# Kernel tuning notes

Hardware: AMD Instinct MI355X
Metric: run time of the kernel (lower is better)

Reference implementation:

```python
import jax, jax.numpy as jnp
import numpy as np

KAPPA = -1.0          # negative curvature (Poincare ball, c = 1)
EPS = 1e-10
N, D_IN, D_OUT = 8192, 512, 512


def _artan_k(x):
    sc = np.sqrt(-KAPPA)
    return jnp.arctanh(jnp.clip(sc * x, -1.0 + 1e-7, 1.0 - 1e-7)) / sc


def _tan_k(x):
    sc = np.sqrt(-KAPPA)
    return jnp.tanh(sc * x) / sc


def _clamp_abs(x, eps=EPS):
    return jnp.where(x >= 0, 1.0, -1.0) * jnp.maximum(jnp.abs(x), eps)


def _norm(x):
    # stable last-dim L2 norm, clamped away from zero
    return jnp.sqrt(jnp.maximum(jnp.sum(x * x, axis=-1, keepdims=True), EPS * EPS))


def mobius_matvec(W, x):
    # geoopt-style Mobius matrix-vector product: scale x@W so that the
    # gyro-norm matches tan_k((|mx|/|x|) * artan_k(|x|))
    x_norm = _norm(x)                       # [N,1]
    mx = x @ W                              # [N,D_out]
    mx_norm = _norm(mx)
    res = _tan_k(mx_norm / x_norm * _artan_k(x_norm)) * (mx / mx_norm)
    return jnp.where(mx_norm <= EPS, 0.0, res)


def mobius_scalar_mul(r, x):
    x_norm = _norm(x)
    return _tan_k(r * _artan_k(x_norm)) * (x / x_norm)


def weighted_midpoint_lincomb(A, X):
    # weighted Frechet-mean-like midpoint with lincomb=True (geoopt semantics):
    # gamma_i = lambda_x = 2 / (1 + kappa * |x_i|^2)
    gamma = jnp.maximum(2.0 / (1.0 + KAPPA * jnp.sum(X * X, axis=-1, keepdims=True)), 1e-15)  # [N,1]
    denom = _clamp_abs(A @ (gamma - 1.0))   # [N,1]  (sum_j A_ij (gamma_j - 1))
    nom = A @ (gamma * X)                   # [N,D]  (sum_j A_ij gamma_j x_j)  -- GEMM, no NxNxD temp
    two_mean = nom / denom
    sq = jnp.sum(two_mean * two_mean, axis=-1, keepdims=True)
    a_mean = two_mean / (1.0 + jnp.sqrt(jnp.maximum(1.0 + KAPPA * sq, EPS)))
    alpha = jnp.sum(A, axis=-1, keepdims=True)   # lincomb: Mobius-scale by total weight
    return mobius_scalar_mul(alpha, a_mean)


def logmap0(x):
    xn = _norm(x)
    return _artan_k(xn) * x / xn


def expmap0(u):
    un = _norm(u)
    return _tan_k(un) * u / un


def setup_inputs() -> dict:
    key = jax.random.key(0)
    k1, k2, k3 = jax.random.split(key, 3)
    # node embeddings well inside the Poincare ball (|x| ~ 0.02)
    X = jax.random.normal(k1, (N, D_IN), dtype=jnp.float32) * 0.001
    # dense nonnegative normalized adjacency (rows sum ~ 0.5)
    A_hat = jax.random.uniform(k2, (N, N), dtype=jnp.float32) / N
    W = jax.random.normal(k3, (D_IN, D_OUT), dtype=jnp.float32) * 0.01
    return {"X": X, "A_hat": A_hat, "W": W}


def reference(X, A_hat, W):
    XW = mobius_matvec(W, X)                     # Mobius linear layer
    AXW = weighted_midpoint_lincomb(A_hat, XW)   # adjacency-weighted midpoint aggregation
    return expmap0(jax.nn.relu(logmap0(AXW)))    # sigma = exp0(relu(log0(.)))
```

## Files before the change

kernel.cpp:

```cpp
#include <hip/hip_runtime.h>


#define NR 8192
#define DD 512

typedef unsigned int u32;
typedef unsigned short u16;
typedef __attribute__((ext_vector_type(8))) short bf16x8;
typedef __attribute__((ext_vector_type(4))) float f32x4;

__device__ __forceinline__ u16 f2bf(float f) {
  u32 u = __float_as_uint(f);
  u32 r = u + 0x7FFFu + ((u >> 16) & 1u);
  return (u16)(r >> 16);
}

__device__ __forceinline__ u32 cvtpk(float lo, float hi) {
  u32 r;
  asm("v_cvt_pk_bf16_f32 %0, %1, %2" : "=v"(r) : "v"(lo), "v"(hi));
  return r;
}

__device__ __forceinline__ void gload16(const void* g, void* l) {
  __builtin_amdgcn_global_load_lds(
      (const __attribute__((address_space(1))) u32*)g,
      (__attribute__((address_space(3))) u32*)l, 16, 0, 0);
}

__device__ __forceinline__ float wred(float v) {
  #pragma unroll
  for (int off = 32; off; off >>= 1) v += __shfl_xor(v, off, 64);
  return v;
}

__global__ __launch_bounds__(256) void conv_wt(const float* __restrict__ W,
                                               u16* __restrict__ Wt) {
  const int idx = blockIdx.x * 256 + threadIdx.x;
  const int n  = idx >> 6;
  const int k0 = (idx & 63) * 8;
  u32 r[4];
  #pragma unroll
  for (int j = 0; j < 4; ++j) {
    float lo = W[(size_t)(k0 + 2*j    ) * DD + n];
    float hi = W[(size_t)(k0 + 2*j + 1) * DD + n];
    r[j] = (u32)f2bf(lo) | ((u32)f2bf(hi) << 16);
  }
  const int dst = n * DD + ((idx & 63) >> 2) * 32 + (((idx & 3) ^ (n & 3)) * 8);
  *(uint4*)(Wt + dst) = *(const uint4*)r;
}

template <int DOSUM>
__global__ __launch_bounds__(256, 2) void gemm_ph(
    const float* __restrict__ Af, const u16* __restrict__ Bt,
    const u16* __restrict__ g1bf,
    float* __restrict__ C0, float* __restrict__ Cext,
    float* __restrict__ denp, float* __restrict__ alp,
    int M, int K, int kchunk, int nkc) {
  __shared__ __align__(16) float ldsA[2][4096];
  __shared__ __align__(16) u16   ldsB[2][8192];
  __shared__ __align__(16) u16   ldsG[4096];

  const int bid = blockIdx.x;
  int mt, nt, kc;
  if (nkc == 4) {
    kc = (bid >> 1) & 3;
    nt = (bid >> 3) & 1;
    mt = ((bid >> 4) << 1) | (bid & 1);
  } else {
    kc = 0;
    nt = bid & 1;
    mt = bid >> 1;
  }

  const int t = threadIdx.x;
  const int lane = t & 63, w = t >> 6;
  const int wm = w >> 1, wn = w & 1;
  const int m0 = mt * 128, n0 = nt * 256;
  const int kbeg = kc * kchunk;
  const int lr = lane & 15, lk = lane >> 4, lx = lr & 7;
  const bool doRS = DOSUM && (nt == 0);

  const int scol = ((t & 7) ^ ((t >> 3) & 7)) << 2;
  const float* gA0 = Af + (size_t)(m0 + (t >> 3)) * K + kbeg + scol;
  const u16* gB = Bt + (size_t)(n0 + (t >> 2)) * K + kbeg + (t & 3) * 8;

  auto stage = [&](int buf, int kt) {
    const int ko = kt * 32;
    #pragma unroll
    for (int j = 0; j < 4; ++j)
      gload16(gA0 + ko + (size_t)j * 32 * K, &ldsA[buf][t * 4 + j * 1024]);
    #pragma unroll
    for (int j = 0; j < 4; ++j)
      gload16(gB + ko + (size_t)j * 64 * K, &ldsB[buf][t * 8 + j * 2048]);
  };

  f32x4 acc[4][8];
  #pragma unroll
  for (int i = 0; i < 4; ++i)
    #pragma unroll
    for (int j = 0; j < 8; ++j) acc[i][j] = (f32x4){0.f, 0.f, 0.f, 0.f};
  f32x4 accS[4];
  #pragma unroll
  for (int i = 0; i < 4; ++i) accS[i] = (f32x4){0.f, 0.f, 0.f, 0.f};

  const int nT = kchunk / 32;

  if (doRS) {
    #pragma unroll
    for (int j = 0; j < 2; ++j)
      gload16(g1bf + kbeg + t * 8 + j * 2048, &ldsG[t * 8 + j * 2048]);
  }
  stage(0, 0);
  stage(1, 1);
  asm volatile("s_waitcnt vmcnt(8)" ::: "memory");
  __builtin_amdgcn_s_barrier();
  __builtin_amdgcn_sched_barrier(0);

  int cur = 0;
  for (int tt = 0; tt < nT; ++tt) {
    bf16x8 af[4], bv[8];
    #pragma unroll
    for (int i = 0; i < 4; ++i) {
      const int rbase = (wm * 64 + i * 16 + lr) * 32;
      f32x4 lo = *(const f32x4*)&ldsA[cur][rbase + (((2*lk    ) ^ lx) << 2)];
      f32x4 hi = *(const f32x4*)&ldsA[cur][rbase + (((2*lk + 1) ^ lx) << 2)];
      union { u32 u[4]; bf16x8 v; } pk;
      pk.u[0] = cvtpk(lo.x, lo.y); pk.u[1] = cvtpk(lo.z, lo.w);
      pk.u[2] = cvtpk(hi.x, hi.y); pk.u[3] = cvtpk(hi.z, hi.w);
      af[i] = pk.v;
    }
    #pragma unroll
    for (int i = 0; i < 8; ++i) {
      const int rb = (wn * 128 + i * 16 + lr) * 32 + ((lk ^ (lr & 3)) << 3);
      bv[i] = *(const bf16x8*)&ldsB[cur][rb];
    }
    __builtin_amdgcn_s_setprio(1);
    #pragma unroll
    for (int mi = 0; mi < 4; ++mi)
      #pragma unroll
      for (int ni = 0; ni < 4; ++ni)
        acc[mi][ni] = __builtin_amdgcn_mfma_f32_16x16x32_bf16(
            af[mi], bv[ni], acc[mi][ni], 0, 0, 0);
    __builtin_amdgcn_s_setprio(0);
    asm volatile("s_waitcnt lgkmcnt(0)" ::: "memory");
    __builtin_amdgcn_sched_barrier(0);
    __builtin_amdgcn_s_barrier();
    __builtin_amdgcn_sched_barrier(0);
    if (tt + 2 < nT) stage(cur, tt + 2);
    bf16x8 gv;
    if (doRS && wn == 0) {
      if (lr == 0) {
        gv = *(const bf16x8*)&ldsG[tt * 32 + lk * 8];
      } else {
        const short s = (lr == 1) ? (short)0x3F80 : (short)0;
        gv = (bf16x8){s, s, s, s, s, s, s, s};
      }
    }
    __builtin_amdgcn_sched_barrier(0);
    __builtin_amdgcn_s_setprio(1);
    #pragma unroll
    for (int mi = 0; mi < 4; ++mi)
      #pragma unroll
      for (int ni = 4; ni < 8; ++ni)
        acc[mi][ni] = __builtin_amdgcn_mfma_f32_16x16x32_bf16(
            af[mi], bv[ni], acc[mi][ni], 0, 0, 0);
    if (doRS && wn == 0) {
      #pragma unroll
      for (int i = 0; i < 4; ++i)
        accS[i] = __builtin_amdgcn_mfma_f32_16x16x32_bf16(
            af[i], gv, accS[i], 0, 0, 0);
    }
    __builtin_amdgcn_s_setprio(0);
    __builtin_amdgcn_sched_barrier(0);
    if (tt + 1 < nT) {
      if (tt + 3 < nT) {
        asm volatile("s_waitcnt vmcnt(8)" ::: "memory");
      } else {
        asm volatile("s_waitcnt vmcnt(0)" ::: "memory");
      }
      __builtin_amdgcn_s_barrier();
      __builtin_amdgcn_sched_barrier(0);
    }
    cur ^= 1;
  }

  if (doRS && wn == 0 && lr < 2) {
    float* dst = ((lr == 0) ? denp : alp) + (size_t)kc * M + m0 + wm * 64;
    #pragma unroll
    for (int i = 0; i < 4; ++i)
      #pragma unroll
      for (int v = 0; v < 4; ++v)
        dst[i * 16 + lk * 4 + v] = accS[i][v];
  }

  float* C = (kc == 0) ? C0 : (Cext + (size_t)(kc - 1) * M * DD);
  float* Cw = C + (size_t)(m0 + wm * 64 + lk * 4) * DD + n0 + wn * 128 + lr;
  #pragma unroll
  for (int mi = 0; mi < 4; ++mi)
    #pragma unroll
    for (int ni = 0; ni < 8; ++ni)
      #pragma unroll
      for (int v = 0; v < 4; ++v)
        Cw[(size_t)(mi * 16 + v) * DD + ni * 16] = acc[mi][ni][v];
}

__global__ __launch_bounds__(256) void rowstats(const float* __restrict__ X,
                                                const float* __restrict__ mx,
                                                float* __restrict__ fg,
                                                u16* __restrict__ g1bf) {
  const int row  = (blockIdx.x << 2) + (threadIdx.x >> 6);
  const int lane = threadIdx.x & 63;
  const float* xr = X  + (size_t)row * DD + lane * 8;
  const float* mr = mx + (size_t)row * DD + lane * 8;
  float4 a0 = *(const float4*)xr, a1 = *(const float4*)(xr + 4);
  float4 b0 = *(const float4*)mr, b1 = *(const float4*)(mr + 4);
  float sx = a0.x*a0.x + a0.y*a0.y + a0.z*a0.z + a0.w*a0.w
           + a1.x*a1.x + a1.y*a1.y + a1.z*a1.z + a1.w*a1.w;
  float sm = b0.x*b0.x + b0.y*b0.y + b0.z*b0.z + b0.w*b0.w
           + b1.x*b1.x + b1.y*b1.y + b1.z*b1.z + b1.w*b1.w;
  sx = wred(sx); sm = wred(sm);
  if (lane == 0) {
    float xn  = sqrtf(fmaxf(sx, 1e-20f));
    float mxn = sqrtf(fmaxf(sm, 1e-20f));
    float at  = atanhf(fminf(xn, 0.9999999f));
    float t_  = tanhf(mxn / xn * at);
    bool  z   = (mxn <= 1e-10f);
    float factor = z ? 0.f : t_ / mxn;
    float xwsq   = z ? 0.f : t_ * t_ * (sm / (mxn * mxn));
    float g = 2.f / (1.f - xwsq);
    g = fmaxf(g, 1e-15f);
    fg[row] = factor * g;
    g1bf[row] = f2bf(g - 1.f);
  }
}

__global__ __launch_bounds__(256) void build_bt(const float* __restrict__ mx,
                                                const float* __restrict__ fg,
                                                u16* __restrict__ Bt) {
  __shared__ float tile[64][65];
  const int j0 = blockIdx.x * 64, d0 = blockIdx.y * 64;
  const int t = threadIdx.x;
  const int r0 = t >> 4, c4 = (t & 15) * 4;
  #pragma unroll
  for (int p = 0; p < 4; ++p) {
    const int r = r0 + p * 16;
    const float s = fg[j0 + r];
    float4 v = *(const float4*)&mx[(size_t)(j0 + r) * DD + d0 + c4];
    tile[r][c4 + 0] = s * v.x; tile[r][c4 + 1] = s * v.y;
    tile[r][c4 + 2] = s * v.z; tile[r][c4 + 3] = s * v.w;
  }
  __syncthreads();
  const int dr = t >> 2, jc = (t & 3) * 16;
  u32 r[8];
  #pragma unroll
  for (int u = 0; u < 8; ++u) {
    float lo = tile[jc + 2 * u][dr];
    float hi = tile[jc + 2 * u + 1][dr];
    r[u] = (u32)f2bf(lo) | ((u32)f2bf(hi) << 16);
  }
  const int s0 = (jc >> 3) & 3;
  const int px = dr & 3;
  u32* rowp = (u32*)(Bt + (size_t)(d0 + dr) * NR + j0 + (jc & 32));
  *(uint4*)(rowp + ((s0 ^ px) * 4))       = *(const uint4*)&r[0];
  *(uint4*)(rowp + (((s0 + 1) ^ px) * 4)) = *(const uint4*)&r[4];
}

__global__ __launch_bounds__(256) void epilogue(const float* __restrict__ P0,
                                                const float* __restrict__ P1,
                                                const float* __restrict__ P2,
                                                const float* __restrict__ P3,
                                                const float* __restrict__ denp,
                                                const float* __restrict__ alp,
                                                float* __restrict__ out) {
  const int row  = (blockIdx.x << 2) + (threadIdx.x >> 6);
  const int lane = threadIdx.x & 63;
  const size_t ro = (size_t)row * DD + lane * 8;
  float4 n0 = *(const float4*)(P0 + ro), n1 = *(const float4*)(P0 + ro + 4);
  float4 a, b;
  a = *(const float4*)(P1 + ro); b = *(const float4*)(P1 + ro + 4);
  n0.x += a.x; n0.y += a.y; n0.z += a.z; n0.w += a.w;
  n1.x += b.x; n1.y += b.y; n1.z += b.z; n1.w += b.w;
  a = *(const float4*)(P2 + ro); b = *(const float4*)(P2 + ro + 4);
  n0.x += a.x; n0.y += a.y; n0.z += a.z; n0.w += a.w;
  n1.x += b.x; n1.y += b.y; n1.z += b.z; n1.w += b.w;
  a = *(const float4*)(P3 + ro); b = *(const float4*)(P3 + ro + 4);
  n0.x += a.x; n0.y += a.y; n0.z += a.z; n0.w += a.w;
  n1.x += b.x; n1.y += b.y; n1.z += b.z; n1.w += b.w;

  float de = 0.f, alpha = 0.f;
  #pragma unroll
  for (int kc = 0; kc < 4; ++kc) {
    de    += denp[kc * NR + row];
    alpha += alp [kc * NR + row];
  }
  de = (de >= 0.f ? 1.f : -1.f) * fmaxf(fabsf(de), 1e-10f);

  float v[8] = {n0.x / de, n0.y / de, n0.z / de, n0.w / de,
                n1.x / de, n1.y / de, n1.z / de, n1.w / de};
  float sq = 0.f;
  #pragma unroll
  for (int j = 0; j < 8; ++j) sq += v[j] * v[j];
  sq = wred(sq);
  float s1 = 1.f + sqrtf(fmaxf(1.f - sq, 1e-10f));
  float an = sqrtf(fmaxf(sq / (s1 * s1), 1e-20f));
  float t2 = tanhf(alpha * atanhf(fminf(an, 0.9999999f)));
  float f2 = t2 / (an * s1);
  float xsq = f2 * f2 * sq;
  float xn = sqrtf(fmaxf(xsq, 1e-20f));
  float lf = atanhf(fminf(xn, 0.9999999f)) / xn;
  float u[8]; float us = 0.f;
  #pragma unroll
  for (int j = 0; j < 8; ++j) {
    u[j] = fmaxf(lf * f2 * v[j], 0.f);
    us += u[j] * u[j];
  }
  us = wred(us);
  float un = sqrtf(fmaxf(us, 1e-20f));
  float ef = tanhf(un) / un;
  float o[8];
  #pragma unroll
  for (int j = 0; j < 8; ++j) o[j] = ef * u[j];
  float* orow = out + (size_t)row * DD + lane * 8;
  *(float4*)orow       = (float4){o[0], o[1], o[2], o[3]};
  *(float4*)(orow + 4) = (float4){o[4], o[5], o[6], o[7]};
}

extern "C" void kernel_launch(void* const* d_in, const int* in_sizes, int n_in,
                              void* d_out, int out_size, void* d_ws, size_t ws_size,
                              hipStream_t stream) {
  const float* X = (const float*)d_in[0];
  const float* A = (const float*)d_in[1];
  const float* W = (const float*)d_in[2];
  float* out = (float*)d_out;
  char* ws = (char*)d_ws;

  float* mx   = (float*)(ws);
  float* Pext = (float*)(ws + 16777216);
  u16*   Bt   = (u16*)(ws + 67108864);
  u16*   Wt   = (u16*)(ws + 75497472);
  float* fg   = (float*)(ws + 76021760);
  u16*   g1bf = (u16*)(ws + 76054528);
  float* denp = (float*)(ws + 76087296);
  float* alp  = (float*)(ws + 76218368);

  const size_t MNf = (size_t)NR * DD;

  conv_wt<<<128, 256, 0, stream>>>(W, Wt);
  gemm_ph<0><<<128, 256, 0, stream>>>(X, Wt, g1bf, mx, mx, denp, alp,
                                      NR, DD, DD, 1);
  rowstats<<<2048, 256, 0, stream>>>(X, mx, fg, g1bf);
  build_bt<<<dim3(128, 8), 256, 0, stream>>>(mx, fg, Bt);
  gemm_ph<1><<<512, 256, 0, stream>>>(A, Bt, g1bf, mx, Pext, denp, alp,
                                      NR, NR, NR / 4, 4);
  epilogue<<<2048, 256, 0, stream>>>(mx, Pext, Pext + MNf, Pext + 2 * MNf,
                                     denp, alp, out);
}
```

Measured before the change: 178.2 us.

## Load fp32 A operand directly into registers and shrink GEMM N-tile to 128

The GEMM kernel stops staging the fp32 A tile through LDS. Each lane now prefetches its own A fragments from global memory into registers, double-buffered, and converts them to bf16 just before the MFMAs. The N tile is halved from 256 to 128, so the grid doubles and the per-wave accumulator footprint and LDS use shrink, which should raise occupancy. In exchange, A is re-read from global memory by twice as many blocks, and the global A loads are less coalesced, 32-byte row segments per lane.

```diff
diff --git a/kernel.cpp b/kernel.cpp
--- a/kernel.cpp
+++ b/kernel.cpp
@@ -50,138 +50,137 @@
 }
 
 template <int DOSUM>
-__global__ __launch_bounds__(256, 2) void gemm_ph(
+__global__ __launch_bounds__(256, 2) void gemm_ra(
     const float* __restrict__ Af, const u16* __restrict__ Bt,
     const u16* __restrict__ g1bf,
     float* __restrict__ C0, float* __restrict__ Cext,
     float* __restrict__ denp, float* __restrict__ alp,
     int M, int K, int kchunk, int nkc) {
-  __shared__ __align__(16) float ldsA[2][4096];
-  __shared__ __align__(16) u16   ldsB[2][8192];
-  __shared__ __align__(16) u16   ldsG[4096];
+  __shared__ __align__(16) u16 ldsB[2][4096];
+  __shared__ __align__(16) u16 ldsG[2048];
 
   const int bid = blockIdx.x;
   int mt, nt, kc;
   if (nkc == 4) {
     kc = (bid >> 1) & 3;
-    nt = (bid >> 3) & 1;
-    mt = ((bid >> 4) << 1) | (bid & 1);
+    nt = (bid >> 3) & 3;
+    mt = ((bid >> 5) << 1) | (bid & 1);
   } else {
     kc = 0;
-    nt = bid & 1;
-    mt = bid >> 1;
+    nt = bid & 3;
+    mt = bid >> 2;
   }
 
   const int t = threadIdx.x;
   const int lane = t & 63, w = t >> 6;
   const int wm = w >> 1, wn = w & 1;
-  const int m0 = mt * 128, n0 = nt * 256;
+  const int m0 = mt * 128, n0 = nt * 128;
   const int kbeg = kc * kchunk;
-  const int lr = lane & 15, lk = lane >> 4, lx = lr & 7;
+  const int lr = lane & 15, lk = lane >> 4;
   const bool doRS = DOSUM && (nt == 0);
-
-  const int scol = ((t & 7) ^ ((t >> 3) & 7)) << 2;
-  const float* gA0 = Af + (size_t)(m0 + (t >> 3)) * K + kbeg + scol;
+  const int nT = kchunk / 32;
+
+  const float* aP[4];
+  #pragma unroll
+  for (int i = 0; i < 4; ++i)
+    aP[i] = Af + (size_t)(m0 + wm * 64 + i * 16 + lr) * K + kbeg + lk * 8;
+
   const u16* gB = Bt + (size_t)(n0 + (t >> 2)) * K + kbeg + (t & 3) * 8;
 
-  auto stage = [&](int buf, int kt) {
-    const int ko = kt * 32;
-    #pragma unroll
-    for (int j = 0; j < 4; ++j)
-      gload16(gA0 + ko + (size_t)j * 32 * K, &ldsA[buf][t * 4 + j * 1024]);
-    #pragma unroll
-    for (int j = 0; j < 4; ++j)
-      gload16(gB + ko + (size_t)j * 64 * K, &ldsB[buf][t * 8 + j * 2048]);
+  float4 pa0[4], pa1[4], pb0[4], pb1[4];
+  auto refill = [&](float4 (&d0)[4], float4 (&d1)[4]) {
+    #pragma unroll
+    for (int i = 0; i < 4; ++i) {
+      d0[i] = *(const float4*)(aP[i]);
+      d1[i] = *(const float4*)(aP[i] + 4);
+      aP[i] += 32;
+    }
   };
 
-  f32x4 acc[4][8];
+  f32x4 acc[4][4];
   #pragma unroll
   for (int i = 0; i < 4; ++i)
     #pragma unroll
-    for (int j = 0; j < 8; ++j) acc[i][j] = (f32x4){0.f, 0.f, 0.f, 0.f};
+    for (int j = 0; j < 4; ++j) acc[i][j] = (f32x4){0.f, 0.f, 0.f, 0.f};
   f32x4 accS[4];
   #pragma unroll
   for (int i = 0; i < 4; ++i) accS[i] = (f32x4){0.f, 0.f, 0.f, 0.f};
 
-  const int nT = kchunk / 32;
-
-  if (doRS) {
-    #pragma unroll
-    for (int j = 0; j < 2; ++j)
-      gload16(g1bf + kbeg + t * 8 + j * 2048, &ldsG[t * 8 + j * 2048]);
-  }
-  stage(0, 0);
-  stage(1, 1);
-  asm volatile("s_waitcnt vmcnt(8)" ::: "memory");
+  if (doRS) gload16(g1bf + kbeg + t * 8, &ldsG[t * 8]);
+  refill(pa0, pa1);
+  refill(pb0, pb1);
+  #pragma unroll
+  for (int j = 0; j < 2; ++j)
+    gload16(gB + (size_t)j * 64 * K, &ldsB[0][t * 8 + j * 2048]);
+  #pragma unroll
+  for (int j = 0; j < 2; ++j)
+    gload16(gB + 32 + (size_t)j * 64 * K, &ldsB[1][t * 8 + j * 2048]);
+  asm volatile("s_waitcnt vmcnt(2)" ::: "memory");
   __builtin_amdgcn_s_barrier();
   __builtin_amdgcn_sched_barrier(0);
 
-  int cur = 0;
-  for (int tt = 0; tt < nT; ++tt) {
-    bf16x8 af[4], bv[8];
+  auto subiter = [&](int T, float4 (&P0)[4], float4 (&P1)[4], u16* bbuf) {
+    bf16x8 bv[4];
+    #pragma unroll
+    for (int i = 0; i < 4; ++i)
+      bv[i] = *(const bf16x8*)
+          &bbuf[(wn * 64 + i * 16 + lr) * 32 + ((lk ^ (lr & 3)) << 3)];
+    bf16x8 gvv;
+    if (doRS && wn == 0) {
+      if (lr == 0) {
+        gvv = *(const bf16x8*)&ldsG[T * 32 + lk * 8];
+      } else {
+        const short s = (lr == 1) ? (short)0x3F80 : (short)0;
+        gvv = (bf16x8){s, s, s, s, s, s, s, s};
+      }
+    }
+    bf16x8 af[4];
     #pragma unroll
     for (int i = 0; i < 4; ++i) {
-      const int rbase = (wm * 64 + i * 16 + lr) * 32;
-      f32x4 lo = *(const f32x4*)&ldsA[cur][rbase + (((2*lk    ) ^ lx) << 2)];
-      f32x4 hi = *(const f32x4*)&ldsA[cur][rbase + (((2*lk + 1) ^ lx) << 2)];
       union { u32 u[4]; bf16x8 v; } pk;
-      pk.u[0] = cvtpk(lo.x, lo.y); pk.u[1] = cvtpk(lo.z, lo.w);
-      pk.u[2] = cvtpk(hi.x, hi.y); pk.u[3] = cvtpk(hi.z, hi.w);
+      pk.u[0] = cvtpk(P0[i].x, P0[i].y); pk.u[1] = cvtpk(P0[i].z, P0[i].w);
+      pk.u[2] = cvtpk(P1[i].x, P1[i].y); pk.u[3] = cvtpk(P1[i].z, P1[i].w);
       af[i] = pk.v;
     }
-    #pragma unroll
-    for (int i = 0; i < 8; ++i) {
-      const int rb = (wn * 128 + i * 16 + lr) * 32 + ((lk ^ (lr & 3)) << 3);
-      bv[i] = *(const bf16x8*)&ldsB[cur][rb];
-    }
-    __builtin_amdgcn_s_setprio(1);
-    #pragma unroll
-    for (int mi = 0; mi < 4; ++mi)
-      #pragma unroll
-      for (int ni = 0; ni < 4; ++ni)
-        acc[mi][ni] = __builtin_amdgcn_mfma_f32_16x16x32_bf16(
-            af[mi], bv[ni], acc[mi][ni], 0, 0, 0);
-    __builtin_amdgcn_s_setprio(0);
+    const bool more = (T + 2 < nT);
+    if (more) refill(P0, P1);
     asm volatile("s_waitcnt lgkmcnt(0)" ::: "memory");
     __builtin_amdgcn_sched_barrier(0);
     __builtin_amdgcn_s_barrier();
     __builtin_amdgcn_sched_barrier(0);
-    if (tt + 2 < nT) stage(cur, tt + 2);
-    bf16x8 gv;
-    if (doRS && wn == 0) {
-      if (lr == 0) {
-        gv = *(const bf16x8*)&ldsG[tt * 32 + lk * 8];
-      } else {
-        const short s = (lr == 1) ? (short)0x3F80 : (short)0;
-        gv = (bf16x8){s, s, s, s, s, s, s, s};
-      }
+    if (more) {
+      const size_t ko = (size_t)(T + 2) * 32;
+      #pragma unroll
+      for (int j = 0; j < 2; ++j)
+        gload16(gB + ko + (size_t)j * 64 * K, &bbuf[t * 8 + j * 2048]);
     }
     __builtin_amdgcn_sched_barrier(0);
     __builtin_amdgcn_s_setprio(1);
     #pragma unroll
     for (int mi = 0; mi < 4; ++mi)
       #pragma unroll
-      for (int ni = 4; ni < 8; ++ni)
+      for (int ni = 0; ni < 4; ++ni)
         acc[mi][ni] = __builtin_amdgcn_mfma_f32_16x16x32_bf16(
             af[mi], bv[ni], acc[mi][ni], 0, 0, 0);
     if (doRS && wn == 0) {
       #pragma unroll
       for (int i = 0; i < 4; ++i)
         accS[i] = __builtin_amdgcn_mfma_f32_16x16x32_bf16(
-            af[i], gv, accS[i], 0, 0, 0);
+            af[i], gvv, accS[i], 0, 0, 0);
     }
     __builtin_amdgcn_s_setprio(0);
     __builtin_amdgcn_sched_barrier(0);
-    if (tt + 1 < nT) {
-      if (tt + 3 < nT) {
-        asm volatile("s_waitcnt vmcnt(8)" ::: "memory");
-      } else {
-        asm volatile("s_waitcnt vmcnt(0)" ::: "memory");
-      }
+    if (T + 1 < nT) {
+      if (more) asm volatile("s_waitcnt vmcnt(10)" ::: "memory");
+      else      asm volatile("s_waitcnt vmcnt(0)"  ::: "memory");
       __builtin_amdgcn_s_barrier();
       __builtin_amdgcn_sched_barrier(0);
     }
-    cur ^= 1;
+  };
+
+  for (int tt = 0; tt < nT; tt += 2) {
+    subiter(tt,     pa0, pa1, &ldsB[0][0]);
+    subiter(tt + 1, pb0, pb1, &ldsB[1][0]);
   }
 
   if (doRS && wn == 0 && lr < 2) {
@@ -194,11 +193,11 @@
   }
 
   float* C = (kc == 0) ? C0 : (Cext + (size_t)(kc - 1) * M * DD);
-  float* Cw = C + (size_t)(m0 + wm * 64 + lk * 4) * DD + n0 + wn * 128 + lr;
+  float* Cw = C + (size_t)(m0 + wm * 64 + lk * 4) * DD + n0 + wn * 64 + lr;
   #pragma unroll
   for (int mi = 0; mi < 4; ++mi)
     #pragma unroll
-    for (int ni = 0; ni < 8; ++ni)
+    for (int ni = 0; ni < 4; ++ni)
       #pragma unroll
       for (int v = 0; v < 4; ++v)
         Cw[(size_t)(mi * 16 + v) * DD + ni * 16] = acc[mi][ni][v];
@@ -346,12 +345,12 @@
   const size_t MNf = (size_t)NR * DD;
 
   conv_wt<<<128, 256, 0, stream>>>(W, Wt);
-  gemm_ph<0><<<128, 256, 0, stream>>>(X, Wt, g1bf, mx, mx, denp, alp,
+  gemm_ra<0><<<256, 256, 0, stream>>>(X, Wt, g1bf, mx, mx, denp, alp,
                                       NR, DD, DD, 1);
   rowstats<<<2048, 256, 0, stream>>>(X, mx, fg, g1bf);
   build_bt<<<dim3(128, 8), 256, 0, stream>>>(mx, fg, Bt);
-  gemm_ph<1><<<512, 256, 0, stream>>>(A, Bt, g1bf, mx, Pext, denp, alp,
-                                      NR, NR, NR / 4, 4);
+  gemm_ra<1><<<1024, 256, 0, stream>>>(A, Bt, g1bf, mx, Pext, denp, alp,
+                                       NR, NR, NR / 4, 4);
   epilogue<<<2048, 256, 0, stream>>>(mx, Pext, Pext + MNf, Pext + 2 * MNf,
                                      denp, alp, out);
 }
```

Result: slower. 352.8 us (+97.9%).

## Use 256x256 tiles with 512-thread blocks and triple-buffered LDS for the adjacency GEMM

Applied to the files above, without the earlier changes.

The large A_hat GEMM moves to a new 512-thread kernel with 256x256 output tiles, 8 waves laid out 2x4, and a three-stage LDS ring. Global-to-LDS prefetch loads are interleaved between the MFMA sub-steps, and block-to-tile mapping is reordered so the K-split index varies fastest. The larger tile is meant to raise data reuse per LDS byte and reduce global traffic for A. The trade is about 148 KB of LDS per block, which leaves one block per CU, and a single wave of 256 blocks. The small X@W GEMM is reduced to a plain double-buffered kernel without the row-sum path or the priority and wait tuning.

```diff
diff --git a/kernel.cpp b/kernel.cpp
--- a/kernel.cpp
+++ b/kernel.cpp
@@ -50,22 +50,22 @@
 }
 
 template <int DOSUM>
-__global__ __launch_bounds__(256, 2) void gemm_ph(
+__global__ __launch_bounds__(512, 2) void gemm8(
     const float* __restrict__ Af, const u16* __restrict__ Bt,
     const u16* __restrict__ g1bf,
     float* __restrict__ C0, float* __restrict__ Cext,
     float* __restrict__ denp, float* __restrict__ alp,
     int M, int K, int kchunk, int nkc) {
-  __shared__ __align__(16) float ldsA[2][4096];
-  __shared__ __align__(16) u16   ldsB[2][8192];
-  __shared__ __align__(16) u16   ldsG[4096];
+  __shared__ __align__(16) float ldsA[3][8192];
+  __shared__ __align__(16) u16   ldsB[3][8192];
+  __shared__ __align__(16) u16   ldsG[2048];
 
   const int bid = blockIdx.x;
   int mt, nt, kc;
   if (nkc == 4) {
-    kc = (bid >> 1) & 3;
+    kc = bid & 3;
     nt = (bid >> 3) & 1;
-    mt = ((bid >> 4) << 1) | (bid & 1);
+    mt = ((bid >> 4) << 1) | ((bid >> 2) & 1);
   } else {
     kc = 0;
     nt = bid & 1;
@@ -74,15 +74,152 @@
 
   const int t = threadIdx.x;
   const int lane = t & 63, w = t >> 6;
-  const int wm = w >> 1, wn = w & 1;
-  const int m0 = mt * 128, n0 = nt * 256;
+  const int wm = w >> 2, wn = w & 3;
+  const int m0 = mt * 256, n0 = nt * 256;
   const int kbeg = kc * kchunk;
   const int lr = lane & 15, lk = lane >> 4, lx = lr & 7;
   const bool doRS = DOSUM && (nt == 0);
+  const int nT = kchunk / 32;
+
+  const int rowA = t >> 3;
+  const int scol = ((t & 7) ^ (rowA & 7)) << 2;
+  const float* gA0 = Af + (size_t)(m0 + rowA) * K + kbeg + scol;
+  const u16* gB = Bt + (size_t)(n0 + (t >> 2)) * K + kbeg + (t & 3) * 8;
+
+  f32x4 acc[8][4];
+  #pragma unroll
+  for (int i = 0; i < 8; ++i)
+    #pragma unroll
+    for (int j = 0; j < 4; ++j) acc[i][j] = (f32x4){0.f, 0.f, 0.f, 0.f};
+  f32x4 accS[8];
+  #pragma unroll
+  for (int i = 0; i < 8; ++i) accS[i] = (f32x4){0.f, 0.f, 0.f, 0.f};
+
+  auto stageA2 = [&](int buf, int kt, int j0) {
+    const int ko = kt * 32;
+    gload16(gA0 + ko + (size_t)(j0    ) * 64 * K, &ldsA[buf][t * 4 + (j0    ) * 2048]);
+    gload16(gA0 + ko + (size_t)(j0 + 1) * 64 * K, &ldsA[buf][t * 4 + (j0 + 1) * 2048]);
+  };
+  auto stageB2 = [&](int buf, int kt) {
+    const int ko = kt * 32;
+    gload16(gB + ko,                    &ldsB[buf][t * 8]);
+    gload16(gB + ko + (size_t)128 * K,  &ldsB[buf][t * 8 + 4096]);
+  };
+
+  if (doRS && t < 256) gload16(g1bf + kbeg + t * 8, &ldsG[t * 8]);
+  stageA2(0, 0, 0); stageA2(0, 0, 2); stageB2(0, 0);
+  stageA2(1, 1, 0); stageA2(1, 1, 2); stageB2(1, 1);
+  asm volatile("s_waitcnt vmcnt(6)" ::: "memory");
+  __builtin_amdgcn_s_barrier();
+  __builtin_amdgcn_sched_barrier(0);
+
+  for (int tt = 0; tt < nT; ++tt) {
+    const int b  = tt % 3;
+    const int sb = (tt + 2) % 3;
+    const bool pf = (tt + 2 < nT);
+    bf16x8 bv[4];
+    #pragma unroll
+    for (int i = 0; i < 4; ++i)
+      bv[i] = *(const bf16x8*)
+          &ldsB[b][(wn * 64 + i * 16 + lr) * 32 + ((lk ^ (lr & 3)) << 3)];
+    bf16x8 gv;
+    if (doRS && wn == 0) {
+      if (lr == 0) {
+        gv = *(const bf16x8*)&ldsG[tt * 32 + lk * 8];
+      } else {
+        const short s = (lr == 1) ? (short)0x3F80 : (short)0;
+        gv = (bf16x8){s, s, s, s, s, s, s, s};
+      }
+    }
+    #pragma unroll
+    for (int p = 0; p < 4; ++p) {
+      bf16x8 afa, afb;
+      {
+        const int ra = (wm * 128 + (2 * p) * 16 + lr) * 32;
+        f32x4 lo = *(const f32x4*)&ldsA[b][ra + (((2 * lk    ) ^ lx) << 2)];
+        f32x4 hi = *(const f32x4*)&ldsA[b][ra + (((2 * lk + 1) ^ lx) << 2)];
+        union { u32 u[4]; bf16x8 v; } pk;
+        pk.u[0] = cvtpk(lo.x, lo.y); pk.u[1] = cvtpk(lo.z, lo.w);
+        pk.u[2] = cvtpk(hi.x, hi.y); pk.u[3] = cvtpk(hi.z, hi.w);
+        afa = pk.v;
+      }
+      {
+        const int ra = (wm * 128 + (2 * p + 1) * 16 + lr) * 32;
+        f32x4 lo = *(const f32x4*)&ldsA[b][ra + (((2 * lk    ) ^ lx) << 2)];
+        f32x4 hi = *(const f32x4*)&ldsA[b][ra + (((2 * lk + 1) ^ lx) << 2)];
+        union { u32 u[4]; bf16x8 v; } pk;
+        pk.u[0] = cvtpk(lo.x, lo.y); pk.u[1] = cvtpk(lo.z, lo.w);
+        pk.u[2] = cvtpk(hi.x, hi.y); pk.u[3] = cvtpk(hi.z, hi.w);
+        afb = pk.v;
+      }
+      if (p == 0 && pf) stageA2(sb, tt + 2, 0);
+      if (p == 1 && pf) stageA2(sb, tt + 2, 2);
+      if (p == 2 && pf) stageB2(sb, tt + 2);
+      __builtin_amdgcn_s_barrier();
+      __builtin_amdgcn_sched_barrier(0);
+      __builtin_amdgcn_s_setprio(1);
+      #pragma unroll
+      for (int ni = 0; ni < 4; ++ni) {
+        acc[2 * p    ][ni] = __builtin_amdgcn_mfma_f32_16x16x32_bf16(
+            afa, bv[ni], acc[2 * p    ][ni], 0, 0, 0);
+        acc[2 * p + 1][ni] = __builtin_amdgcn_mfma_f32_16x16x32_bf16(
+            afb, bv[ni], acc[2 * p + 1][ni], 0, 0, 0);
+      }
+      if (doRS && wn == 0) {
+        accS[2 * p    ] = __builtin_amdgcn_mfma_f32_16x16x32_bf16(
+            afa, gv, accS[2 * p    ], 0, 0, 0);
+        accS[2 * p + 1] = __builtin_amdgcn_mfma_f32_16x16x32_bf16(
+            afb, gv, accS[2 * p + 1], 0, 0, 0);
+      }
+      __builtin_amdgcn_s_setprio(0);
+      __builtin_amdgcn_sched_barrier(0);
+      if (p == 3 && tt + 1 < nT) {
+        if (pf) asm volatile("s_waitcnt vmcnt(6)" ::: "memory");
+        else    asm volatile("s_waitcnt vmcnt(0)" ::: "memory");
+      }
+      __builtin_amdgcn_s_barrier();
+      __builtin_amdgcn_sched_barrier(0);
+    }
+  }
+
+  if (doRS && wn == 0 && lr < 2) {
+    float* dst = ((lr == 0) ? denp : alp) + (size_t)kc * M + m0 + wm * 128;
+    #pragma unroll
+    for (int i = 0; i < 8; ++i)
+      #pragma unroll
+      for (int v = 0; v < 4; ++v)
+        dst[i * 16 + lk * 4 + v] = accS[i][v];
+  }
+
+  float* C = (kc == 0) ? C0 : (Cext + (size_t)(kc - 1) * M * DD);
+  float* Cw = C + (size_t)(m0 + wm * 128 + lk * 4) * DD + n0 + wn * 64 + lr;
+  #pragma unroll
+  for (int mi = 0; mi < 8; ++mi)
+    #pragma unroll
+    for (int ni = 0; ni < 4; ++ni)
+      #pragma unroll
+      for (int v = 0; v < 4; ++v)
+        Cw[(size_t)(mi * 16 + v) * DD + ni * 16] = acc[mi][ni][v];
+}
+
+__global__ __launch_bounds__(256, 2) void gemm_ph(
+    const float* __restrict__ Af, const u16* __restrict__ Bt,
+    float* __restrict__ C0, int M, int K) {
+  __shared__ __align__(16) float ldsA[2][4096];
+  __shared__ __align__(16) u16   ldsB[2][8192];
+  const int bid = blockIdx.x;
+  const int nt = bid & 1;
+  const int mt = bid >> 1;
+
+  const int t = threadIdx.x;
+  const int lane = t & 63, w = t >> 6;
+  const int wm = w >> 1, wn = w & 1;
+  const int m0 = mt * 128, n0 = nt * 256;
+  const int lr = lane & 15, lk = lane >> 4, lx = lr & 7;
 
   const int scol = ((t & 7) ^ ((t >> 3) & 7)) << 2;
-  const float* gA0 = Af + (size_t)(m0 + (t >> 3)) * K + kbeg + scol;
-  const u16* gB = Bt + (size_t)(n0 + (t >> 2)) * K + kbeg + (t & 3) * 8;
+  const float* gA0 = Af + (size_t)(m0 + (t >> 3)) * K + scol;
+  const u16* gB = Bt + (size_t)(n0 + (t >> 2)) * K + (t & 3) * 8;
 
   auto stage = [&](int buf, int kt) {
     const int ko = kt * 32;
@@ -99,25 +236,13 @@
   for (int i = 0; i < 4; ++i)
     #pragma unroll
     for (int j = 0; j < 8; ++j) acc[i][j] = (f32x4){0.f, 0.f, 0.f, 0.f};
-  f32x4 accS[4];
-  #pragma unroll
-  for (int i = 0; i < 4; ++i) accS[i] = (f32x4){0.f, 0.f, 0.f, 0.f};
-
-  const int nT = kchunk / 32;
-
-  if (doRS) {
-    #pragma unroll
-    for (int j = 0; j < 2; ++j)
-      gload16(g1bf + kbeg + t * 8 + j * 2048, &ldsG[t * 8 + j * 2048]);
-  }
+
+  const int nT = K / 32;
   stage(0, 0);
-  stage(1, 1);
-  asm volatile("s_waitcnt vmcnt(8)" ::: "memory");
-  __builtin_amdgcn_s_barrier();
-  __builtin_amdgcn_sched_barrier(0);
-
-  int cur = 0;
+  __syncthreads();
   for (int tt = 0; tt < nT; ++tt) {
+    const int cur = tt & 1;
+    if (tt + 1 < nT) stage(cur ^ 1, tt + 1);
     bf16x8 af[4], bv[8];
     #pragma unroll
     for (int i = 0; i < 4; ++i) {
@@ -134,67 +259,16 @@
       const int rb = (wn * 128 + i * 16 + lr) * 32 + ((lk ^ (lr & 3)) << 3);
       bv[i] = *(const bf16x8*)&ldsB[cur][rb];
     }
-    __builtin_amdgcn_s_setprio(1);
     #pragma unroll
     for (int mi = 0; mi < 4; ++mi)
       #pragma unroll
-      for (int ni = 0; ni < 4; ++ni)
+      for (int ni = 0; ni < 8; ++ni)
         acc[mi][ni] = __builtin_amdgcn_mfma_f32_16x16x32_bf16(
             af[mi], bv[ni], acc[mi][ni], 0, 0, 0);
-    __builtin_amdgcn_s_setprio(0);
-    asm volatile("s_waitcnt lgkmcnt(0)" ::: "memory");
-    __builtin_amdgcn_sched_barrier(0);
-    __builtin_amdgcn_s_barrier();
-    __builtin_amdgcn_sched_barrier(0);
-    if (tt + 2 < nT) stage(cur, tt + 2);
-    bf16x8 gv;
-    if (doRS && wn == 0) {
-      if (lr == 0) {
-        gv = *(const bf16x8*)&ldsG[tt * 32 + lk * 8];
-      } else {
-        const short s = (lr == 1) ? (short)0x3F80 : (short)0;
-        gv = (bf16x8){s, s, s, s, s, s, s, s};
-      }
-    }
-    __builtin_amdgcn_sched_barrier(0);
-    __builtin_amdgcn_s_setprio(1);
-    #pragma unroll
-    for (int mi = 0; mi < 4; ++mi)
-      #pragma unroll
-      for (int ni = 4; ni < 8; ++ni)
-        acc[mi][ni] = __builtin_amdgcn_mfma_f32_16x16x32_bf16(
-            af[mi], bv[ni], acc[mi][ni], 0, 0, 0);
-    if (doRS && wn == 0) {
-      #pragma unroll
-      for (int i = 0; i < 4; ++i)
-        accS[i] = __builtin_amdgcn_mfma_f32_16x16x32_bf16(
-            af[i], gv, accS[i], 0, 0, 0);
-    }
-    __builtin_amdgcn_s_setprio(0);
-    __builtin_amdgcn_sched_barrier(0);
-    if (tt + 1 < nT) {
-      if (tt + 3 < nT) {
-        asm volatile("s_waitcnt vmcnt(8)" ::: "memory");
-      } else {
-        asm volatile("s_waitcnt vmcnt(0)" ::: "memory");
-      }
-      __builtin_amdgcn_s_barrier();
-      __builtin_amdgcn_sched_barrier(0);
-    }
-    cur ^= 1;
-  }
-
-  if (doRS && wn == 0 && lr < 2) {
-    float* dst = ((lr == 0) ? denp : alp) + (size_t)kc * M + m0 + wm * 64;
-    #pragma unroll
-    for (int i = 0; i < 4; ++i)
-      #pragma unroll
-      for (int v = 0; v < 4; ++v)
-        dst[i * 16 + lk * 4 + v] = accS[i][v];
-  }
-
-  float* C = (kc == 0) ? C0 : (Cext + (size_t)(kc - 1) * M * DD);
-  float* Cw = C + (size_t)(m0 + wm * 64 + lk * 4) * DD + n0 + wn * 128 + lr;
+    __syncthreads();
+  }
+
+  float* Cw = C0 + (size_t)(m0 + wm * 64 + lk * 4) * DD + n0 + wn * 128 + lr;
   #pragma unroll
   for (int mi = 0; mi < 4; ++mi)
     #pragma unroll
@@ -346,12 +420,11 @@
   const size_t MNf = (size_t)NR * DD;
 
   conv_wt<<<128, 256, 0, stream>>>(W, Wt);
-  gemm_ph<0><<<128, 256, 0, stream>>>(X, Wt, g1bf, mx, mx, denp, alp,
-                                      NR, DD, DD, 1);
+  gemm_ph<<<128, 256, 0, stream>>>(X, Wt, mx, NR, DD);
   rowstats<<<2048, 256, 0, stream>>>(X, mx, fg, g1bf);
   build_bt<<<dim3(128, 8), 256, 0, stream>>>(mx, fg, Bt);
-  gemm_ph<1><<<512, 256, 0, stream>>>(A, Bt, g1bf, mx, Pext, denp, alp,
-                                      NR, NR, NR / 4, 4);
+  gemm8<1><<<256, 512, 0, stream>>>(A, Bt, g1bf, mx, Pext, denp, alp,
+                                    NR, NR, NR / 4, 4);
   epilogue<<<2048, 256, 0, stream>>>(mx, Pext, Pext + MNf, Pext + 2 * MNf,
                                      denp, alp, out);
 }
```

Result: slower. 220.7 us (+23.8%).
